# Performance work log

Measured on AMD Instinct MI355X. Metric: run time of the kernel, lower is better.

## Reference

```python
import jax, jax.numpy as jnp
import numpy as np

B, T, N, D = 8, 192, 64, 512
H = 8
DH = D // H
C = 8


def setup_inputs() -> dict:
    key = jax.random.key(0)
    ks = jax.random.split(key, 10)
    s = 1.0 / np.sqrt(D)
    return {
        "x": jax.random.normal(ks[0], (B, T, N, D), dtype=jnp.float32),
        "Wq_w": jax.random.normal(ks[1], (D, D), dtype=jnp.float32) * s,
        "Wq_b": jnp.zeros((D,), dtype=jnp.float32),
        "Wv_w": jax.random.normal(ks[2], (D, D), dtype=jnp.float32) * s,
        "Wv_b": jnp.zeros((D,), dtype=jnp.float32),
        "Wk": jax.random.normal(ks[3], (C, D, D), dtype=jnp.float32) * s,
        "bk": jnp.zeros((C, D), dtype=jnp.float32),
        "proj_w": jax.random.normal(ks[4], (D, D), dtype=jnp.float32) * s,
        "proj_b": jnp.zeros((D,), dtype=jnp.float32),
        "cluster_ids": jax.random.randint(ks[5], (N,), 0, C, dtype=jnp.int64),
    }


def reference(x, Wq_w, Wq_b, Wv_w, Wv_b, Wk, bk, proj_w, proj_b, cluster_ids):
    # torch Linear: y = x @ W.T + b
    Q = jnp.einsum('btnd,ed->btne', x, Wq_w) + Wq_b
    V = jnp.einsum('btnd,ed->btne', x, Wv_w) + Wv_b
    # per-cluster K projection == per-node weight gather (grouped GEMM)
    Wk_n = Wk[cluster_ids]          # [N, D, D]
    bk_n = bk[cluster_ids]          # [N, D]
    K = jnp.einsum('btnd,nde->btne', x, Wk_n) + bk_n

    def split_heads(z):
        # [B,T,N,D] -> [B,N,H,T,DH]
        return z.reshape(B, T, N, H, DH).transpose(0, 2, 3, 1, 4)

    Qh, Kh, Vh = split_heads(Q), split_heads(K), split_heads(V)
    scores = jnp.einsum('bnhtd,bnhsd->bnhts', Qh, Kh) / np.sqrt(DH).astype(np.float32)
    attn = jax.nn.softmax(scores, axis=-1)
    out_h = jnp.einsum('bnhts,bnhsd->bnhtd', attn, Vh)
    out = out_h.transpose(0, 3, 1, 2, 4).reshape(B, T, N, D)
    return jnp.einsum('btnd,ed->btne', out, proj_w) + proj_b
```

## Files before the change

### kernel.cpp

```cpp
#include <hip/hip_runtime.h>
#include <hip/hip_bf16.h>

typedef __bf16 bf16x8 __attribute__((ext_vector_type(8)));
typedef float  f32x4  __attribute__((ext_vector_type(4)));

#define MFMA16(a, b, c) __builtin_amdgcn_mfma_f32_16x16x32_bf16(a, b, c, 0, 0, 0)

__device__ __forceinline__ void async16(const __bf16* g, __bf16* l) {
    __builtin_amdgcn_global_load_lds(
        (const __attribute__((address_space(1))) unsigned int*)g,
        (__attribute__((address_space(3))) unsigned int*)l, 16, 0, 0);
}


__global__ void k_cast3(const float* __restrict__ wq, const float* __restrict__ wv,
                        const float* __restrict__ wp,
                        __bf16* __restrict__ oq, __bf16* __restrict__ ov,
                        __bf16* __restrict__ op) {
    int i = blockIdx.x * 256 + threadIdx.x;
    oq[i] = (__bf16)wq[i];
    ov[i] = (__bf16)wv[i];
    op[i] = (__bf16)wp[i];
}

__global__ void k_twk(const float* __restrict__ wk, __bf16* __restrict__ o) {
    int i = blockIdx.x * 256 + threadIdx.x;
    int c = i >> 18;
    int r = i & 262143;
    int d = r >> 9;
    int e = r & 511;
    o[(c << 18) + (e << 9) + d] = (__bf16)wk[i];
}

__global__ void k_castx(const float* __restrict__ x, __bf16* __restrict__ o) {
    size_t i = ((size_t)blockIdx.x * 256 + threadIdx.x) * 8;
    float4 f0 = *(const float4*)(x + i);
    float4 f1 = *(const float4*)(x + i + 4);
    bf16x8 v;
    v[0] = (__bf16)f0.x; v[1] = (__bf16)f0.y; v[2] = (__bf16)f0.z; v[3] = (__bf16)f0.w;
    v[4] = (__bf16)f1.x; v[5] = (__bf16)f1.y; v[6] = (__bf16)f1.z; v[7] = (__bf16)f1.w;
    *(bf16x8*)(o + i) = v;
}

__launch_bounds__(512, 2)
__global__ void k_qkv(const __bf16* __restrict__ xb,
                      const __bf16* __restrict__ WqE, const __bf16* __restrict__ WvE,
                      const __bf16* __restrict__ WkE,
                      const float* __restrict__ bq, const float* __restrict__ bv,
                      const float* __restrict__ bk, const int* __restrict__ cid,
                      __bf16* __restrict__ Qw, __bf16* __restrict__ Kw,
                      __bf16* __restrict__ Vw) {
    const int g   = blockIdx.y * 36 + blockIdx.x;
    const int s   = (g & 7) * 288 + (g >> 3);
    const int n   = s / 36;
    const int r36 = s - n * 36;
    const int mx  = r36 / 6;
    const int ey  = r36 - mx * 6;
    const int m0  = mx * 256;
    const int e0  = ey * 256;
    const int seg  = e0 >> 9;
    const int eoff = e0 & 511;
    const int c    = cid[n];

    const __bf16* Wb = (seg == 0) ? WqE : (seg == 1) ? WvE : (WkE + ((size_t)c << 18));
    __bf16*       Ob = (seg == 0) ? Qw : (seg == 1) ? Vw : Kw;

    __shared__ __align__(16) __bf16 Ar[4][256 * 32];
    __shared__ __align__(16) __bf16 Br[4][256 * 32];

    const int tid  = threadIdx.x;
    const int lane = tid & 63;
    const int w    = tid >> 6;
    const int wm2  = w >> 2;
    const int wn4  = w & 3;
    const int l15  = lane & 15, qd = lane >> 4;

    const int sr  = tid >> 2;
    const int sp  = tid & 3;
    const int sch = (sp ^ ((sr >> 1) & 3)) * 8;
    const __bf16* aG0 = xb + ((size_t)(m0 + sr) * 64 + n) * 512 + sch;
    const __bf16* aG1 = aG0 + (size_t)128 * 64 * 512;
    const __bf16* bG0 = Wb + ((size_t)(eoff + sr) << 9) + sch;
    const __bf16* bG1 = bG0 + ((size_t)128 << 9);

    const int cro   = (qd ^ ((l15 >> 1) & 3)) * 8;
    const int arow0 = (wm2 * 128 + l15) * 32;
    const int brow0 = (wn4 * 64 + l15) * 32;

    f32x4 acc[8][4];
#pragma unroll
    for (int i = 0; i < 8; ++i)
#pragma unroll
        for (int j = 0; j < 4; ++j) acc[i][j] = (f32x4){0.f, 0.f, 0.f, 0.f};

    auto issue = [&](int t) {
        const int slot = t & 3;
        const int k0 = t * 32;
        __bf16* ad = &Ar[slot][tid * 8];
        __bf16* bd = &Br[slot][tid * 8];
        async16(aG0 + k0, ad);
        async16(aG1 + k0, ad + 4096);
        async16(bG0 + k0, bd);
        async16(bG1 + k0, bd + 4096);
    };
    auto compute = [&](int slot) {
        const __bf16* Asl = Ar[slot];
        const __bf16* Bsl = Br[slot];
        bf16x8 bfr[4], af[8];
#pragma unroll
        for (int j = 0; j < 4; ++j)
            bfr[j] = *(const bf16x8*)&Bsl[brow0 + j * 512 + cro];
#pragma unroll
        for (int i = 0; i < 8; ++i)
            af[i] = *(const bf16x8*)&Asl[arow0 + i * 512 + cro];
        __builtin_amdgcn_s_setprio(1);
#pragma unroll
        for (int i = 0; i < 8; ++i)
#pragma unroll
            for (int j = 0; j < 4; ++j)
                acc[i][j] = MFMA16(af[i], bfr[j], acc[i][j]);
        __builtin_amdgcn_s_setprio(0);
    };

    issue(0); issue(1); issue(2);
    asm volatile("s_waitcnt vmcnt(8)" ::: "memory");
    __builtin_amdgcn_s_barrier();

    for (int t = 0; t < 13; ++t) {
        issue(t + 3);
        compute(t & 3);
        asm volatile("s_waitcnt vmcnt(8)" ::: "memory");
        __builtin_amdgcn_s_barrier();
    }
    compute(1);
    asm volatile("s_waitcnt vmcnt(4)" ::: "memory");
    __builtin_amdgcn_s_barrier();
    compute(2);
    asm volatile("s_waitcnt vmcnt(0)" ::: "memory");
    __builtin_amdgcn_s_barrier();
    compute(3);

    float bias[4];
#pragma unroll
    for (int j = 0; j < 4; ++j) {
        int e = eoff + wn4 * 64 + j * 16 + l15;
        bias[j] = (seg == 0) ? bq[e] : (seg == 1) ? bv[e] : bk[(c << 9) + e];
    }
#pragma unroll
    for (int i = 0; i < 8; ++i) {
#pragma unroll
        for (int rx = 0; rx < 4; ++rx) {
            int m  = m0 + wm2 * 128 + i * 16 + qd * 4 + rx;
            int bb = m / 192;
            int tt = m - bb * 192;
            size_t ro = ((size_t)(bb * 64 + n) * 192 + tt) << 9;
#pragma unroll
            for (int j = 0; j < 4; ++j) {
                int e = eoff + wn4 * 64 + j * 16 + l15;
                Ob[ro + e] = (__bf16)(acc[i][j][rx] + bias[j]);
            }
        }
    }
}

__launch_bounds__(768)
__global__ void k_attn(const __bf16* __restrict__ Qw, const __bf16* __restrict__ Kw,
                       const __bf16* __restrict__ Vw, __bf16* __restrict__ Ow) {
    const int h = blockIdx.x, n = blockIdx.y, b = blockIdx.z;
    __shared__ __align__(16) __bf16 Ks[192 * 72];
    __shared__ __align__(16) __bf16 Vt[64 * 192];
    __shared__ __align__(16) __bf16 Ps[192 * 200];

    const int tid  = threadIdx.x;
    const int lane = tid & 63, w = tid >> 6;
    const int l15  = lane & 15, qd = lane >> 4;
    const size_t base = ((size_t)((b * 64 + n) * 192) << 9) + h * 64;

    for (int i = tid; i < 1536; i += 768) {
        int row = i >> 3, pp = i & 7;
        *(bf16x8*)&Ks[row * 72 + 8 * pp] =
            *(const bf16x8*)(Kw + base + ((size_t)row << 9) + 8 * pp);
    }
#pragma unroll
    for (int rr = 0; rr < 2; ++rr) {
        int idx = rr * 768 + tid;
        int e = idx & 63, sb = idx >> 6;
        bf16x8 v;
#pragma unroll
        for (int j = 0; j < 8; ++j)
            v[j] = Vw[base + (size_t)(sb * 8 + j) * 512 + e];
        *(bf16x8*)&Vt[e * 192 + ((sb ^ (e & 7)) * 8)] = v;
    }
    __syncthreads();

    const __bf16* qp = Qw + base + ((size_t)(16 * w + l15) << 9) + 8 * qd;
    bf16x8 aq0 = *(const bf16x8*)(qp);
    bf16x8 aq1 = *(const bf16x8*)(qp + 32);

    f32x4 S[12];
#pragma unroll
    for (int ct = 0; ct < 12; ++ct) {
        f32x4 acc = (f32x4){0.f, 0.f, 0.f, 0.f};
        bf16x8 b0 = *(const bf16x8*)&Ks[(16 * ct + l15) * 72 + 8 * qd];
        bf16x8 b1 = *(const bf16x8*)&Ks[(16 * ct + l15) * 72 + 32 + 8 * qd];
        acc = MFMA16(aq0, b0, acc);
        acc = MFMA16(aq1, b1, acc);
        S[ct] = acc;
    }

    float mx[4] = {-1e30f, -1e30f, -1e30f, -1e30f};
#pragma unroll
    for (int ct = 0; ct < 12; ++ct)
#pragma unroll
        for (int rx = 0; rx < 4; ++rx) mx[rx] = fmaxf(mx[rx], S[ct][rx]);
#pragma unroll
    for (int mk = 1; mk < 16; mk <<= 1)
#pragma unroll
        for (int rx = 0; rx < 4; ++rx) mx[rx] = fmaxf(mx[rx], __shfl_xor(mx[rx], mk, 64));

    const float sc = 0.125f * 1.44269504088896f;
    float sm[4] = {0.f, 0.f, 0.f, 0.f};
#pragma unroll
    for (int ct = 0; ct < 12; ++ct) {
#pragma unroll
        for (int rx = 0; rx < 4; ++rx) {
            float pe = exp2f((S[ct][rx] - mx[rx]) * sc);
            sm[rx] += pe;
            Ps[(w * 16 + qd * 4 + rx) * 200 + 16 * ct + l15] = (__bf16)pe;
        }
    }
#pragma unroll
    for (int mk = 1; mk < 16; mk <<= 1)
#pragma unroll
        for (int rx = 0; rx < 4; ++rx) sm[rx] += __shfl_xor(sm[rx], mk, 64);

    __syncthreads();

    float inv[4];
#pragma unroll
    for (int rx = 0; rx < 4; ++rx) inv[rx] = 1.f / sm[rx];

#pragma unroll
    for (int et = 0; et < 4; ++et) {
        f32x4 acc = (f32x4){0.f, 0.f, 0.f, 0.f};
#pragma unroll
        for (int sn = 0; sn < 6; ++sn) {
            bf16x8 pa = *(const bf16x8*)&Ps[(w * 16 + l15) * 200 + sn * 32 + 8 * qd];
            bf16x8 vb = *(const bf16x8*)
                &Vt[(et * 16 + l15) * 192 + (((sn * 4 + qd) ^ (l15 & 7)) * 8)];
            acc = MFMA16(pa, vb, acc);
        }
#pragma unroll
        for (int rx = 0; rx < 4; ++rx) {
            int t = 16 * w + 4 * qd + rx;
            Ow[base + ((size_t)t << 9) + et * 16 + l15] = (__bf16)(acc[rx] * inv[rx]);
        }
    }
}

__launch_bounds__(512, 2)
__global__ void k_proj(const __bf16* __restrict__ Ow, const __bf16* __restrict__ WpE,
                       const float* __restrict__ bp, float* __restrict__ out) {
    const int g   = blockIdx.x;
    const int s   = (g & 7) * 96 + (g >> 3);
    const int n   = s / 12;
    const int r12 = s - n * 12;
    const int mx  = r12 >> 1;
    const int ey  = r12 & 1;
    const int m0  = mx * 256;
    const int e0  = ey * 256;

    __shared__ __align__(16) __bf16 Ar[4][256 * 32];
    __shared__ __align__(16) __bf16 Br[4][256 * 32];

    const int tid  = threadIdx.x;
    const int lane = tid & 63;
    const int w    = tid >> 6;
    const int wm2  = w >> 2;
    const int wn4  = w & 3;
    const int l15  = lane & 15, qd = lane >> 4;

    const int sr  = tid >> 2;
    const int sp  = tid & 3;
    const int sch = (sp ^ ((sr >> 1) & 3)) * 8;
    int mA0 = m0 + sr;       int bb0 = mA0 / 192, tt0 = mA0 - bb0 * 192;
    int mA1 = m0 + 128 + sr; int bb1 = mA1 / 192, tt1 = mA1 - bb1 * 192;
    const __bf16* aG0 = Ow + (((size_t)(bb0 * 64 + n) * 192 + tt0) << 9) + sch;
    const __bf16* aG1 = Ow + (((size_t)(bb1 * 64 + n) * 192 + tt1) << 9) + sch;
    const __bf16* bG0 = WpE + ((size_t)(e0 + sr) << 9) + sch;
    const __bf16* bG1 = bG0 + ((size_t)128 << 9);

    const int cro   = (qd ^ ((l15 >> 1) & 3)) * 8;
    const int arow0 = (wm2 * 128 + l15) * 32;
    const int brow0 = (wn4 * 64 + l15) * 32;

    f32x4 acc[8][4];
#pragma unroll
    for (int i = 0; i < 8; ++i)
#pragma unroll
        for (int j = 0; j < 4; ++j) acc[i][j] = (f32x4){0.f, 0.f, 0.f, 0.f};

    auto issue = [&](int t) {
        const int slot = t & 3;
        const int k0 = t * 32;
        __bf16* ad = &Ar[slot][tid * 8];
        __bf16* bd = &Br[slot][tid * 8];
        async16(aG0 + k0, ad);
        async16(aG1 + k0, ad + 4096);
        async16(bG0 + k0, bd);
        async16(bG1 + k0, bd + 4096);
    };
    auto compute = [&](int slot) {
        const __bf16* Asl = Ar[slot];
        const __bf16* Bsl = Br[slot];
        bf16x8 bfr[4], af[8];
#pragma unroll
        for (int j = 0; j < 4; ++j)
            bfr[j] = *(const bf16x8*)&Bsl[brow0 + j * 512 + cro];
#pragma unroll
        for (int i = 0; i < 8; ++i)
            af[i] = *(const bf16x8*)&Asl[arow0 + i * 512 + cro];
        __builtin_amdgcn_s_setprio(1);
#pragma unroll
        for (int i = 0; i < 8; ++i)
#pragma unroll
            for (int j = 0; j < 4; ++j)
                acc[i][j] = MFMA16(af[i], bfr[j], acc[i][j]);
        __builtin_amdgcn_s_setprio(0);
    };

    issue(0); issue(1); issue(2);
    asm volatile("s_waitcnt vmcnt(8)" ::: "memory");
    __builtin_amdgcn_s_barrier();

    for (int t = 0; t < 13; ++t) {
        issue(t + 3);
        compute(t & 3);
        asm volatile("s_waitcnt vmcnt(8)" ::: "memory");
        __builtin_amdgcn_s_barrier();
    }
    compute(1);
    asm volatile("s_waitcnt vmcnt(4)" ::: "memory");
    __builtin_amdgcn_s_barrier();
    compute(2);
    asm volatile("s_waitcnt vmcnt(0)" ::: "memory");
    __builtin_amdgcn_s_barrier();
    compute(3);

    float bias[4];
#pragma unroll
    for (int j = 0; j < 4; ++j) bias[j] = bp[e0 + wn4 * 64 + j * 16 + l15];
#pragma unroll
    for (int i = 0; i < 8; ++i) {
#pragma unroll
        for (int rx = 0; rx < 4; ++rx) {
            int m = m0 + wm2 * 128 + i * 16 + qd * 4 + rx;
            size_t ro = ((size_t)(m * 64 + n)) << 9;
#pragma unroll
            for (int j = 0; j < 4; ++j) {
                int e = e0 + wn4 * 64 + j * 16 + l15;
                out[ro + e] = acc[i][j][rx] + bias[j];
            }
        }
    }
}

extern "C" void kernel_launch(void* const* d_in, const int* in_sizes, int n_in,
                              void* d_out, int out_size, void* d_ws, size_t ws_size,
                              hipStream_t stream) {
    const float* x    = (const float*)d_in[0];
    const float* Wq_w = (const float*)d_in[1];
    const float* Wq_b = (const float*)d_in[2];
    const float* Wv_w = (const float*)d_in[3];
    const float* Wv_b = (const float*)d_in[4];
    const float* Wk   = (const float*)d_in[5];
    const float* bk   = (const float*)d_in[6];
    const float* Wp   = (const float*)d_in[7];
    const float* bp   = (const float*)d_in[8];
    const int*   cid  = (const int*)d_in[9];
    float* out = (float*)d_out;

    __bf16* WqE = (__bf16*)d_ws;
    __bf16* WvE = WqE + (1 << 18);
    __bf16* WpE = WvE + (1 << 18);
    __bf16* WkE = WpE + (1 << 18);
    __bf16* Qw  = WkE + (8 << 18);
    __bf16* Kw  = Qw + 50331648LL;
    __bf16* Vw  = Kw + 50331648LL;
    __bf16* XO  = Vw + 50331648LL;

    k_cast3<<<1024, 256, 0, stream>>>(Wq_w, Wv_w, Wp, WqE, WvE, WpE);
    k_twk<<<8192, 256, 0, stream>>>(Wk, WkE);
    k_castx<<<24576, 256, 0, stream>>>(x, XO);
    k_qkv<<<dim3(36, 64), 512, 0, stream>>>(XO, WqE, WvE, WkE, Wq_b, Wv_b, bk, cid,
                                            Qw, Kw, Vw);
    k_attn<<<dim3(8, 64, 8), 768, 0, stream>>>(Qw, Kw, Vw, XO);
    k_proj<<<768, 512, 0, stream>>>(XO, WpE, bp, out);
}
```

Before: 783.6 us.

## Keep softmax probabilities in registers for PV MFMA; tile Wk transpose via LDS

The attention kernel now computes S transposed (K as the A operand), so each lane holds a column of scores. The probabilities are packed to bf16 in registers and fed straight into a 16x16x16 MFMA as the A operand, which removes the Ps shared-memory buffer, its writes and reads, and a block barrier. The row reductions shrink to two cross-lane shuffles. Separately, the Wk transpose/cast kernel uses 64x64 LDS tiles with vector loads and stores instead of scattered 2-byte writes, trading a smaller grid for coalesced access.

```diff
diff --git a/kernel.cpp b/kernel.cpp
--- a/kernel.cpp
+++ b/kernel.cpp
@@ -3,8 +3,10 @@
 
 typedef __bf16 bf16x8 __attribute__((ext_vector_type(8)));
 typedef float  f32x4  __attribute__((ext_vector_type(4)));
+typedef short  s16x4  __attribute__((ext_vector_type(4)));
 
 #define MFMA16(a, b, c) __builtin_amdgcn_mfma_f32_16x16x32_bf16(a, b, c, 0, 0, 0)
+#define MFMA16K16(a, b, c) __builtin_amdgcn_mfma_f32_16x16x16bf16_1k(a, b, c, 0, 0, 0)
 
 __device__ __forceinline__ void async16(const __bf16* g, __bf16* l) {
     __builtin_amdgcn_global_load_lds(
@@ -24,12 +26,37 @@
 }
 
 __global__ void k_twk(const float* __restrict__ wk, __bf16* __restrict__ o) {
-    int i = blockIdx.x * 256 + threadIdx.x;
-    int c = i >> 18;
-    int r = i & 262143;
-    int d = r >> 9;
-    int e = r & 511;
-    o[(c << 18) + (e << 9) + d] = (__bf16)wk[i];
+    const int blk = blockIdx.x;
+    const int c  = blk >> 6;
+    const int dt = (blk >> 3) & 7;
+    const int et = blk & 7;
+    __shared__ __bf16 T[64][72];
+    const int tid = threadIdx.x;
+    {
+        const int rd = tid >> 2;
+        const int ce = (tid & 3) * 16;
+        const float* src = wk + ((size_t)c << 18) + ((size_t)(dt * 64 + rd) << 9)
+                         + et * 64 + ce;
+#pragma unroll
+        for (int q = 0; q < 4; ++q) {
+            float4 f = *(const float4*)(src + q * 4);
+            T[rd][ce + q * 4 + 0] = (__bf16)f.x;
+            T[rd][ce + q * 4 + 1] = (__bf16)f.y;
+            T[rd][ce + q * 4 + 2] = (__bf16)f.z;
+            T[rd][ce + q * 4 + 3] = (__bf16)f.w;
+        }
+    }
+    __syncthreads();
+    {
+        const int re = tid >> 2;
+        const int cd = (tid & 3) * 16;
+        bf16x8 v0, v1;
+#pragma unroll
+        for (int j = 0; j < 8; ++j) { v0[j] = T[cd + j][re]; v1[j] = T[cd + 8 + j][re]; }
+        __bf16* dst = o + ((size_t)c << 18) + ((size_t)(et * 64 + re) << 9) + dt * 64 + cd;
+        *(bf16x8*)dst = v0;
+        *(bf16x8*)(dst + 8) = v1;
+    }
 }
 
 __global__ void k_castx(const float* __restrict__ x, __bf16* __restrict__ o) {
@@ -169,7 +196,6 @@
     const int h = blockIdx.x, n = blockIdx.y, b = blockIdx.z;
     __shared__ __align__(16) __bf16 Ks[192 * 72];
     __shared__ __align__(16) __bf16 Vt[64 * 192];
-    __shared__ __align__(16) __bf16 Ps[192 * 200];
 
     const int tid  = threadIdx.x;
     const int lane = tid & 63, w = tid >> 6;
@@ -203,57 +229,61 @@
         f32x4 acc = (f32x4){0.f, 0.f, 0.f, 0.f};
         bf16x8 b0 = *(const bf16x8*)&Ks[(16 * ct + l15) * 72 + 8 * qd];
         bf16x8 b1 = *(const bf16x8*)&Ks[(16 * ct + l15) * 72 + 32 + 8 * qd];
-        acc = MFMA16(aq0, b0, acc);
-        acc = MFMA16(aq1, b1, acc);
+        acc = MFMA16(b0, aq0, acc);
+        acc = MFMA16(b1, aq1, acc);
         S[ct] = acc;
     }
 
-    float mx[4] = {-1e30f, -1e30f, -1e30f, -1e30f};
+    float mx = -1e30f;
 #pragma unroll
     for (int ct = 0; ct < 12; ++ct)
 #pragma unroll
-        for (int rx = 0; rx < 4; ++rx) mx[rx] = fmaxf(mx[rx], S[ct][rx]);
-#pragma unroll
-    for (int mk = 1; mk < 16; mk <<= 1)
-#pragma unroll
-        for (int rx = 0; rx < 4; ++rx) mx[rx] = fmaxf(mx[rx], __shfl_xor(mx[rx], mk, 64));
+        for (int rx = 0; rx < 4; ++rx) mx = fmaxf(mx, S[ct][rx]);
+    mx = fmaxf(mx, __shfl_xor(mx, 16, 64));
+    mx = fmaxf(mx, __shfl_xor(mx, 32, 64));
 
     const float sc = 0.125f * 1.44269504088896f;
-    float sm[4] = {0.f, 0.f, 0.f, 0.f};
+    float sm = 0.f;
+#pragma unroll
+    for (int ct = 0; ct < 12; ++ct)
+#pragma unroll
+        for (int rx = 0; rx < 4; ++rx) {
+            float pe = exp2f((S[ct][rx] - mx) * sc);
+            S[ct][rx] = pe;
+            sm += pe;
+        }
+    sm += __shfl_xor(sm, 16, 64);
+    sm += __shfl_xor(sm, 32, 64);
+    const float inv = 1.f / sm;
+
+    unsigned pk0[12], pk1[12];
 #pragma unroll
     for (int ct = 0; ct < 12; ++ct) {
-#pragma unroll
-        for (int rx = 0; rx < 4; ++rx) {
-            float pe = exp2f((S[ct][rx] - mx[rx]) * sc);
-            sm[rx] += pe;
-            Ps[(w * 16 + qd * 4 + rx) * 200 + 16 * ct + l15] = (__bf16)pe;
-        }
-    }
-#pragma unroll
-    for (int mk = 1; mk < 16; mk <<= 1)
-#pragma unroll
-        for (int rx = 0; rx < 4; ++rx) sm[rx] += __shfl_xor(sm[rx], mk, 64);
-
-    __syncthreads();
-
-    float inv[4];
-#pragma unroll
-    for (int rx = 0; rx < 4; ++rx) inv[rx] = 1.f / sm[rx];
+        asm("v_cvt_pk_bf16_f32 %0, %1, %2" : "=v"(pk0[ct]) : "v"(S[ct][0]), "v"(S[ct][1]));
+        asm("v_cvt_pk_bf16_f32 %0, %1, %2" : "=v"(pk1[ct]) : "v"(S[ct][2]), "v"(S[ct][3]));
+    }
+
+    float invr[4];
+#pragma unroll
+    for (int rx = 0; rx < 4; ++rx) invr[rx] = __shfl(inv, qd * 4 + rx, 64);
 
 #pragma unroll
     for (int et = 0; et < 4; ++et) {
         f32x4 acc = (f32x4){0.f, 0.f, 0.f, 0.f};
 #pragma unroll
-        for (int sn = 0; sn < 6; ++sn) {
-            bf16x8 pa = *(const bf16x8*)&Ps[(w * 16 + l15) * 200 + sn * 32 + 8 * qd];
-            bf16x8 vb = *(const bf16x8*)
-                &Vt[(et * 16 + l15) * 192 + (((sn * 4 + qd) ^ (l15 & 7)) * 8)];
-            acc = MFMA16(pa, vb, acc);
+        for (int sn = 0; sn < 12; ++sn) {
+            union { unsigned u[2]; s16x4 s; } pa;
+            pa.u[0] = pk0[sn];
+            pa.u[1] = pk1[sn];
+            const int sb = sn * 2 + (qd >> 1);
+            s16x4 vb = *(const s16x4*)
+                &Vt[(et * 16 + l15) * 192 + ((sb ^ (l15 & 7)) * 8) + (qd & 1) * 4];
+            acc = MFMA16K16(pa.s, vb, acc);
         }
 #pragma unroll
         for (int rx = 0; rx < 4; ++rx) {
             int t = 16 * w + 4 * qd + rx;
-            Ow[base + ((size_t)t << 9) + et * 16 + l15] = (__bf16)(acc[rx] * inv[rx]);
+            Ow[base + ((size_t)t << 9) + et * 16 + l15] = (__bf16)(acc[rx] * invr[rx]);
         }
     }
 }
@@ -390,7 +420,7 @@
     __bf16* XO  = Vw + 50331648LL;
 
     k_cast3<<<1024, 256, 0, stream>>>(Wq_w, Wv_w, Wp, WqE, WvE, WpE);
-    k_twk<<<8192, 256, 0, stream>>>(Wk, WkE);
+    k_twk<<<512, 256, 0, stream>>>(Wk, WkE);
     k_castx<<<24576, 256, 0, stream>>>(x, XO);
     k_qkv<<<dim3(36, 64), 512, 0, stream>>>(XO, WqE, WvE, WkE, Wq_b, Wv_b, bk, cid,
                                             Qw, Kw, Vw);
```

Result: faster. 754.2 us (-3.7%).
